# Performance work log

Measured on AMD Instinct MI355X. Metric: run time of the kernel, lower is better.

The kernel has to match this reference:

```python
import jax, jax.numpy as jnp
import numpy as np

N = 100000      # nodes
E = 1600000     # edges
IN = 64         # in_feats
H = 64          # h_feats
L = 4           # num_conv_layers
FC = 2          # num_fc_layers
G = 512         # num graphs in batch
EPS = 1e-5      # BatchNorm eps


def _bn(x, g, b):
    # training-mode BatchNorm1d: batch stats (biased variance), affine
    m = x.mean(axis=0)
    v = x.var(axis=0)
    return (x - m) * jax.lax.rsqrt(v + EPS) * g + b


def setup_inputs() -> dict:
    key = jax.random.key(0)
    ks = jax.random.split(key, 12)
    x = jax.random.normal(ks[0], (N, IN), jnp.float32)
    edge_index = jax.random.randint(ks[1], (2, E), 0, N)
    batch = jnp.sort(jax.random.randint(ks[2], (N,), 0, G))
    s_in = 1.0 / np.sqrt(IN)
    s_h = 1.0 / np.sqrt(H)
    return {
        "x": x,
        "edge_index": edge_index,
        "batch": batch,
        "bn_feat_g": jnp.ones((IN,), jnp.float32),
        "bn_feat_b": jnp.zeros((IN,), jnp.float32),
        "lin_feat_W": jax.random.normal(ks[3], (IN, H), jnp.float32) * s_in,
        "lin_feat_b": jnp.zeros((H,), jnp.float32),
        "bn_conv_g": jnp.ones((L, H), jnp.float32),
        "bn_conv_b": jnp.zeros((L, H), jnp.float32),
        "conv_W": jax.random.normal(ks[4], (L, H, H), jnp.float32) * s_h,
        "conv_b": jnp.zeros((L, H), jnp.float32),
        "bn_fc_g": jnp.ones((FC, H), jnp.float32),
        "bn_fc_b": jnp.zeros((FC, H), jnp.float32),
        "fc_W": jax.random.normal(ks[5], (FC, H, H), jnp.float32) * s_h,
        "fc_b": jnp.zeros((FC, H), jnp.float32),
        "bn_hid_g": jnp.ones((H,), jnp.float32),
        "bn_hid_b": jnp.zeros((H,), jnp.float32),
    }


def reference(x, edge_index, batch, bn_feat_g, bn_feat_b, lin_feat_W, lin_feat_b,
              bn_conv_g, bn_conv_b, conv_W, conv_b, bn_fc_g, bn_fc_b, fc_W, fc_b,
              bn_hid_g, bn_hid_b):
    # --- GCN symmetric normalization with self-loops (computed once) ---
    loop = jnp.arange(N)
    src = jnp.concatenate([edge_index[0], loop])   # source j
    dst = jnp.concatenate([edge_index[1], loop])   # target i
    deg = jax.ops.segment_sum(jnp.ones((E + N,), x.dtype), dst, num_segments=N)
    dinv = jnp.where(deg > 0, 1.0, 0.0) / jnp.sqrt(jnp.where(deg > 0, deg, 1.0))
    norm = dinv[src] * dinv[dst]                   # [E+N]

    # --- stem ---
    h = _bn(x, bn_feat_g, bn_feat_b)
    h = jax.nn.relu(h @ lin_feat_W + lin_feat_b)

    # --- stacked GCNConv + BN + ReLU + residual ---
    for i in range(L):
        h_ = _bn(h, bn_conv_g[i], bn_conv_b[i])
        m = h_ @ conv_W[i]                                    # [N,H]
        agg = jax.ops.segment_sum(norm[:, None] * m[src], dst, num_segments=N)
        h = h + jax.nn.relu(agg + conv_b[i])                  # residual=True

    # --- global add pool over graphs ---
    h = jax.ops.segment_sum(h, batch, num_segments=G)         # [G,H]

    # --- fc head ---
    for i in range(FC):
        h_ = _bn(h, bn_fc_g[i], bn_fc_b[i])
        h = jax.nn.relu(h_ @ fc_W[i] + fc_b[i])

    return _bn(h, bn_hid_g, bn_hid_b)
```

## Files before the change

### kernel.cpp

```cpp
#include <hip/hip_runtime.h>
#include <hip/hip_fp16.h>

#define NN 100000
#define EE 1600000
#define GG 512
#define NB ((NN + 255) / 256)

__global__ void deg_kernel(const int* __restrict__ ei, int* __restrict__ cnt, int E_) {
    int e = blockIdx.x * 256 + threadIdx.x;
    if (e < E_) atomicAdd(&cnt[ei[E_ + e]], 1);
}

__global__ void dinv_kernel(const int* __restrict__ cnt, float* __restrict__ dinv, int n) {
    int i = blockIdx.x * 256 + threadIdx.x;
    if (i < n) dinv[i] = rsqrtf((float)cnt[i] + 1.0f);
}

__global__ void blocksum(const int* __restrict__ cnt, int* __restrict__ bsum) {
    __shared__ int sh[256];
    int i = blockIdx.x * 256 + threadIdx.x;
    sh[threadIdx.x] = (i < NN) ? cnt[i] : 0;
    __syncthreads();
    for (int o = 128; o > 0; o >>= 1) {
        if (threadIdx.x < o) sh[threadIdx.x] += sh[threadIdx.x + o];
        __syncthreads();
    }
    if (threadIdx.x == 0) bsum[blockIdx.x] = sh[0];
}

__global__ void scan_bsum(int* __restrict__ bsum, int nb) {
    __shared__ int sh[512];
    int t = threadIdx.x;
    int v = (t < nb) ? bsum[t] : 0;
    int orig = v;
    sh[t] = v;
    __syncthreads();
    for (int o = 1; o < 512; o <<= 1) {
        int add = (t >= o) ? sh[t - o] : 0;
        __syncthreads();
        sh[t] += add;
        __syncthreads();
    }
    if (t < nb) bsum[t] = sh[t] - orig;
}

__global__ void scan_final(const int* __restrict__ cnt, const int* __restrict__ boff,
                           int* __restrict__ row_ptr, int* __restrict__ cursor) {
    __shared__ int sh[256];
    int i = blockIdx.x * 256 + threadIdx.x;
    int v = (i < NN) ? cnt[i] : 0;
    int orig = v;
    sh[threadIdx.x] = v;
    __syncthreads();
    for (int o = 1; o < 256; o <<= 1) {
        int add = (threadIdx.x >= o) ? sh[threadIdx.x - o] : 0;
        __syncthreads();
        sh[threadIdx.x] += add;
        __syncthreads();
    }
    if (i < NN) {
        int ex = boff[blockIdx.x] + sh[threadIdx.x] - orig;
        row_ptr[i] = ex;
        cursor[i] = ex;
    }
    if (i == 0) row_ptr[NN] = EE;
}

__global__ void fill_csr(const int* __restrict__ ei, const float* __restrict__ dinv,
                         int* __restrict__ cursor, int* __restrict__ csr_src,
                         float* __restrict__ csr_norm, int E_) {
    int e = blockIdx.x * 256 + threadIdx.x;
    if (e < E_) {
        int s = ei[e], d = ei[E_ + e];
        int pos = atomicAdd(&cursor[d], 1);
        csr_src[pos] = s;
        csr_norm[pos] = dinv[s] * dinv[d];
    }
}

__global__ void colstats(const float* __restrict__ A, int nrows, float* __restrict__ stats) {
    __shared__ float ssum[4][64];
    __shared__ float ssq[4][64];
    int tid = threadIdx.x;
    int col = tid & 63, rg = tid >> 6;
    float s = 0.f, q = 0.f;
    for (int r = blockIdx.x * 4 + rg; r < nrows; r += gridDim.x * 4) {
        float v = A[r * 64 + col];
        s += v;
        q = fmaf(v, v, q);
    }
    ssum[rg][col] = s; ssq[rg][col] = q;
    __syncthreads();
    if (tid < 64) {
        float ts = ssum[0][tid] + ssum[1][tid] + ssum[2][tid] + ssum[3][tid];
        float tq = ssq[0][tid] + ssq[1][tid] + ssq[2][tid] + ssq[3][tid];
        atomicAdd(&stats[tid], ts);
        atomicAdd(&stats[64 + tid], tq);
    }
}

__global__ void prep(const float* __restrict__ stats, float count,
                     const float* __restrict__ g, const float* __restrict__ b,
                     const float* __restrict__ W, const float* __restrict__ basebias,
                     float* __restrict__ Wp, float* __restrict__ bp) {
    int j = threadIdx.x;
    float acc = basebias ? basebias[j] : 0.f;
    for (int k = 0; k < 64; k++) {
        float mu  = stats[k] / count;
        float var = fmaxf(stats[64 + k] / count - mu * mu, 0.f);
        float rstd = rsqrtf(var + 1e-5f);
        float a = rstd * g[k];
        float w = W[k * 64 + j];
        Wp[k * 64 + j] = a * w;
        acc = fmaf(b[k] - mu * a, w, acc);
    }
    bp[j] = acc;
}

__global__ __launch_bounds__(256) void gemm64(const float* __restrict__ A,
                                              const float* __restrict__ Wp,
                                              const float* __restrict__ bp,
                                              float* __restrict__ C,
                                              __half* __restrict__ C16,
                                              int nrows, int dorelu,
                                              float* __restrict__ stats) {
    __shared__ float Ws[64 * 64];
    __shared__ float As[64 * 64];
    __shared__ float ssh[256];
    __shared__ float qsh[256];
    int tid = threadIdx.x;
    int row0 = blockIdx.x * 64;
    for (int i = tid; i < 4096; i += 256) {
        Ws[i] = Wp[i];
        int r = row0 + (i >> 6);
        As[i] = (r < nrows) ? A[row0 * 64 + i] : 0.f;
    }
    __syncthreads();
    int col = tid & 63;
    int rg = tid >> 6;
    float bcol = bp[col];
    float s = 0.f, q = 0.f;
    for (int rr = rg; rr < 64; rr += 4) {
        int r = row0 + rr;
        if (r >= nrows) break;
        float acc = bcol;
#pragma unroll
        for (int k = 0; k < 64; k++) acc = fmaf(As[rr * 64 + k], Ws[k * 64 + col], acc);
        float v = dorelu ? fmaxf(acc, 0.f) : acc;
        if (C)   C[r * 64 + col] = v;
        if (C16) C16[r * 64 + col] = __float2half(v);
        s += v;
        q = fmaf(v, v, q);
    }
    if (stats) {
        ssh[tid] = s; qsh[tid] = q;
        __syncthreads();
        if (tid < 64) {
            float ts = ssh[tid] + ssh[64 + tid] + ssh[128 + tid] + ssh[192 + tid];
            float tq = qsh[tid] + qsh[64 + tid] + qsh[128 + tid] + qsh[192 + tid];
            atomicAdd(&stats[tid], ts);
            atomicAdd(&stats[64 + tid], tq);
        }
    }
}

__device__ __forceinline__ void row4(const __half* __restrict__ base, int cl,
                                     float& x, float& y, float& z, float& w) {
    uint2 raw = ((const uint2*)base)[cl];
    __half2 h01 = *reinterpret_cast<const __half2*>(&raw.x);
    __half2 h23 = *reinterpret_cast<const __half2*>(&raw.y);
    float2 f01 = __half22float2(h01);
    float2 f23 = __half22float2(h23);
    x = f01.x; y = f01.y; z = f23.x; w = f23.y;
}

__global__ __launch_bounds__(256) void gather(const int* __restrict__ row_ptr,
                                              const int* __restrict__ csr_src,
                                              const float* __restrict__ csr_norm,
                                              const float* __restrict__ dinv,
                                              const __half* __restrict__ m,
                                              float* __restrict__ h,
                                              const float* __restrict__ cb,
                                              float* __restrict__ stats,
                                              float* __restrict__ pooled,
                                              const int* __restrict__ batch,
                                              int writeH) {
    int tid = threadIdx.x;
    int ng = tid >> 4;
    int cl = tid & 15;
    const float4* cb4 = (const float4*)cb;
    float4 cbv = cb4[cl];
    float sx = 0.f, sy = 0.f, sz = 0.f, sw = 0.f;
    float qx = 0.f, qy = 0.f, qz = 0.f, qw = 0.f;
    for (int i = blockIdx.x * 16 + ng; i < NN; i += gridDim.x * 16) {
        float di = dinv[i];
        float mx, my, mz, mw;
        row4(m + (size_t)i * 64, cl, mx, my, mz, mw);
        float d2 = di * di;
        float ax = d2 * mx, ay = d2 * my, az = d2 * mz, aw = d2 * mw;
        int e0 = row_ptr[i], e1 = row_ptr[i + 1];
        int e = e0;
        for (; e + 3 < e1; e += 4) {
            int s0 = csr_src[e + 0];
            int s1 = csr_src[e + 1];
            int s2 = csr_src[e + 2];
            int s3 = csr_src[e + 3];
            float w0 = csr_norm[e + 0];
            float w1 = csr_norm[e + 1];
            float w2 = csr_norm[e + 2];
            float w3 = csr_norm[e + 3];
            float x0, y0, z0, w0v, x1, y1, z1, w1v, x2, y2, z2, w2v, x3, y3, z3, w3v;
            row4(m + (size_t)s0 * 64, cl, x0, y0, z0, w0v);
            row4(m + (size_t)s1 * 64, cl, x1, y1, z1, w1v);
            row4(m + (size_t)s2 * 64, cl, x2, y2, z2, w2v);
            row4(m + (size_t)s3 * 64, cl, x3, y3, z3, w3v);
            ax = fmaf(w0, x0, ax); ay = fmaf(w0, y0, ay);
            az = fmaf(w0, z0, az); aw = fmaf(w0, w0v, aw);
            ax = fmaf(w1, x1, ax); ay = fmaf(w1, y1, ay);
            az = fmaf(w1, z1, az); aw = fmaf(w1, w1v, aw);
            ax = fmaf(w2, x2, ax); ay = fmaf(w2, y2, ay);
            az = fmaf(w2, z2, az); aw = fmaf(w2, w2v, aw);
            ax = fmaf(w3, x3, ax); ay = fmaf(w3, y3, ay);
            az = fmaf(w3, z3, az); aw = fmaf(w3, w3v, aw);
        }
        for (; e < e1; e++) {
            int s = csr_src[e];
            float w = csr_norm[e];
            float xs, ys, zs, wsv;
            row4(m + (size_t)s * 64, cl, xs, ys, zs, wsv);
            ax = fmaf(w, xs, ax);
            ay = fmaf(w, ys, ay);
            az = fmaf(w, zs, az);
            aw = fmaf(w, wsv, aw);
        }
        float4 hb = ((const float4*)(h + (size_t)i * 64))[cl];
        float nx = hb.x + fmaxf(ax + cbv.x, 0.f);
        float ny = hb.y + fmaxf(ay + cbv.y, 0.f);
        float nz = hb.z + fmaxf(az + cbv.z, 0.f);
        float nw = hb.w + fmaxf(aw + cbv.w, 0.f);
        if (writeH) {
            float4 o; o.x = nx; o.y = ny; o.z = nz; o.w = nw;
            ((float4*)(h + (size_t)i * 64))[cl] = o;
        }
        if (stats) {
            sx += nx; sy += ny; sz += nz; sw += nw;
            qx = fmaf(nx, nx, qx); qy = fmaf(ny, ny, qy);
            qz = fmaf(nz, nz, qz); qw = fmaf(nw, nw, qw);
        }
        if (pooled) {
            int g = batch[i];
            float* p = pooled + g * 64 + cl * 4;
            atomicAdd(p + 0, nx);
            atomicAdd(p + 1, ny);
            atomicAdd(p + 2, nz);
            atomicAdd(p + 3, nw);
        }
    }
    if (stats) {
        __shared__ float rs[256 * 4];
        __shared__ float rq[256 * 4];
        rs[tid * 4 + 0] = sx; rs[tid * 4 + 1] = sy; rs[tid * 4 + 2] = sz; rs[tid * 4 + 3] = sw;
        rq[tid * 4 + 0] = qx; rq[tid * 4 + 1] = qy; rq[tid * 4 + 2] = qz; rq[tid * 4 + 3] = qw;
        __syncthreads();
        if (tid < 64) {
            int cl2 = tid >> 2, k = tid & 3;
            float a = 0.f, b = 0.f;
            for (int g = 0; g < 16; g++) {
                a += rs[(g * 16 + cl2) * 4 + k];
                b += rq[(g * 16 + cl2) * 4 + k];
            }
            atomicAdd(&stats[tid], a);
            atomicAdd(&stats[64 + tid], b);
        }
    }
}

__global__ void bn_apply(const float* __restrict__ A, const float* __restrict__ stats, float count,
                         const float* __restrict__ g, const float* __restrict__ b,
                         float* __restrict__ out, int total) {
    int idx = blockIdx.x * 256 + threadIdx.x;
    if (idx < total) {
        int j = idx & 63;
        float mu  = stats[j] / count;
        float var = fmaxf(stats[64 + j] / count - mu * mu, 0.f);
        float rstd = rsqrtf(var + 1e-5f);
        out[idx] = (A[idx] - mu) * rstd * g[j] + b[j];
    }
}

extern "C" void kernel_launch(void* const* d_in, const int* in_sizes, int n_in,
                              void* d_out, int out_size, void* d_ws, size_t ws_size,
                              hipStream_t stream) {
    const float* x     = (const float*)d_in[0];
    const int*   ei    = (const int*)d_in[1];
    const int*   batch = (const int*)d_in[2];
    const float* bnfg  = (const float*)d_in[3];
    const float* bnfb  = (const float*)d_in[4];
    const float* linW  = (const float*)d_in[5];
    const float* linb  = (const float*)d_in[6];
    const float* bncg  = (const float*)d_in[7];
    const float* bncb  = (const float*)d_in[8];
    const float* convW = (const float*)d_in[9];
    const float* convb = (const float*)d_in[10];
    const float* bnfcg = (const float*)d_in[11];
    const float* bnfcb = (const float*)d_in[12];
    const float* fcW   = (const float*)d_in[13];
    const float* fcb   = (const float*)d_in[14];
    const float* bnhg  = (const float*)d_in[15];
    const float* bnhb  = (const float*)d_in[16];

    const int N64 = NN * 64;
    float* ws = (float*)d_ws;
    size_t o = 0;
    int*   cnt      = (int*)(ws + o);   o += 100352;
    float* dinv     = ws + o;           o += 100352;
    int*   row_ptr  = (int*)(ws + o);   o += 100352;
    int*   cursor   = (int*)(ws + o);   o += 100352;
    int*   bsum     = (int*)(ws + o);   o += 512;
    int*   csr_src  = (int*)(ws + o);   o += EE;
    float* csr_norm = ws + o;           o += EE;
    float* h        = ws + o;           o += N64;
    __half* m16     = (__half*)(ws + o); o += N64 / 2;
    float* statsA   = ws + o;           o += 128;
    float* statsB   = ws + o;           o += 128;
    float* Wp       = ws + o;           o += 4096;
    float* bp       = ws + o;           o += 64;
    float* pa       = ws + o;           o += GG * 64;
    float* pb       = ws + o;           o += GG * 64;

    hipMemsetAsync(cnt, 0, NN * sizeof(int), stream);
    deg_kernel<<<(EE + 255) / 256, 256, 0, stream>>>(ei, cnt, EE);
    dinv_kernel<<<NB, 256, 0, stream>>>(cnt, dinv, NN);
    blocksum<<<NB, 256, 0, stream>>>(cnt, bsum);
    scan_bsum<<<1, 512, 0, stream>>>(bsum, NB);
    scan_final<<<NB, 256, 0, stream>>>(cnt, bsum, row_ptr, cursor);
    fill_csr<<<(EE + 255) / 256, 256, 0, stream>>>(ei, dinv, cursor, csr_src, csr_norm, EE);

    hipMemsetAsync(statsA, 0, 512, stream);
    colstats<<<256, 256, 0, stream>>>(x, NN, statsA);
    prep<<<1, 64, 0, stream>>>(statsA, (float)NN, bnfg, bnfb, linW, linb, Wp, bp);
    hipMemsetAsync(statsB, 0, 512, stream);
    gemm64<<<(NN + 63) / 64, 256, 0, stream>>>(x, Wp, bp, h, nullptr, NN, 1, statsB);

    hipMemsetAsync(pa, 0, GG * 64 * sizeof(float), stream);
    float* cur = statsB; float* nxt = statsA;
    for (int l = 0; l < 4; l++) {
        prep<<<1, 64, 0, stream>>>(cur, (float)NN, bncg + 64 * l, bncb + 64 * l,
                                   convW + 4096 * l, nullptr, Wp, bp);
        gemm64<<<(NN + 63) / 64, 256, 0, stream>>>(h, Wp, bp, nullptr, m16, NN, 0, nullptr);
        if (l < 3) {
            hipMemsetAsync(nxt, 0, 512, stream);
            gather<<<2048, 256, 0, stream>>>(row_ptr, csr_src, csr_norm, dinv, m16, h,
                                             convb + 64 * l, nxt, nullptr, batch, 1);
        } else {
            gather<<<2048, 256, 0, stream>>>(row_ptr, csr_src, csr_norm, dinv, m16, h,
                                             convb + 64 * l, nullptr, pa, batch, 0);
        }
        float* t = cur; cur = nxt; nxt = t;
    }

    float* pin = pa; float* pout = pb;
    for (int i = 0; i < 2; i++) {
        hipMemsetAsync(statsA, 0, 512, stream);
        colstats<<<8, 256, 0, stream>>>(pin, GG, statsA);
        prep<<<1, 64, 0, stream>>>(statsA, (float)GG, bnfcg + 64 * i, bnfcb + 64 * i,
                                   fcW + 4096 * i, fcb + 64 * i, Wp, bp);
        gemm64<<<(GG + 63) / 64, 256, 0, stream>>>(pin, Wp, bp, pout, nullptr, GG, 1, nullptr);
        float* t = pin; pin = pout; pout = t;
    }

    hipMemsetAsync(statsA, 0, 512, stream);
    colstats<<<8, 256, 0, stream>>>(pin, GG, statsA);
    bn_apply<<<(GG * 64 + 255) / 256, 256, 0, stream>>>(pin, statsA, (float)GG, bnhg, bnhb,
                                                        (float*)d_out, GG * 64);
}
```

Baseline: 1.147 ms.

## Fuse BN prep into GEMM, store hidden state in fp16, drop csr_norm

Folds the BatchNorm-into-weights prep step into the GEMM kernel, so every block recomputes the scale and shift and the bias fold, and seven tiny single-block launches go away. The residual hidden state h is kept in fp16 instead of fp32, which halves its read/write traffic in the gather and GEMM kernels. The per-edge csr_norm array is dropped and recomputed in the gather as dinv[i]*dinv[src], trading a streamed array for an extra random gather. The cost is lower precision in the residual accumulation, more redundant work in each GEMM block, and extra random dinv reads.

```diff
diff --git a/kernel.cpp b/kernel.cpp
--- a/kernel.cpp
+++ b/kernel.cpp
@@ -66,15 +66,13 @@
     if (i == 0) row_ptr[NN] = EE;
 }
 
-__global__ void fill_csr(const int* __restrict__ ei, const float* __restrict__ dinv,
-                         int* __restrict__ cursor, int* __restrict__ csr_src,
-                         float* __restrict__ csr_norm, int E_) {
+__global__ void fill_csr(const int* __restrict__ ei, int* __restrict__ cursor,
+                         int* __restrict__ csr_src, int E_) {
     int e = blockIdx.x * 256 + threadIdx.x;
     if (e < E_) {
         int s = ei[e], d = ei[E_ + e];
         int pos = atomicAdd(&cursor[d], 1);
         csr_src[pos] = s;
-        csr_norm[pos] = dinv[s] * dinv[d];
     }
 }
 
@@ -99,46 +97,67 @@
     }
 }
 
-__global__ void prep(const float* __restrict__ stats, float count,
-                     const float* __restrict__ g, const float* __restrict__ b,
-                     const float* __restrict__ W, const float* __restrict__ basebias,
-                     float* __restrict__ Wp, float* __restrict__ bp) {
-    int j = threadIdx.x;
-    float acc = basebias ? basebias[j] : 0.f;
-    for (int k = 0; k < 64; k++) {
-        float mu  = stats[k] / count;
-        float var = fmaxf(stats[64 + k] / count - mu * mu, 0.f);
-        float rstd = rsqrtf(var + 1e-5f);
-        float a = rstd * g[k];
-        float w = W[k * 64 + j];
-        Wp[k * 64 + j] = a * w;
-        acc = fmaf(b[k] - mu * a, w, acc);
-    }
-    bp[j] = acc;
-}
-
-__global__ __launch_bounds__(256) void gemm64(const float* __restrict__ A,
-                                              const float* __restrict__ Wp,
-                                              const float* __restrict__ bp,
-                                              float* __restrict__ C,
-                                              __half* __restrict__ C16,
-                                              int nrows, int dorelu,
-                                              float* __restrict__ stats) {
+__global__ __launch_bounds__(256) void gemm64f(const float* __restrict__ A32,
+                                               const __half* __restrict__ A16,
+                                               const float* __restrict__ W,
+                                               const float* __restrict__ g,
+                                               const float* __restrict__ b,
+                                               const float* __restrict__ basebias,
+                                               const float* __restrict__ statsIn, float count,
+                                               float* __restrict__ C32,
+                                               __half* __restrict__ C16,
+                                               int nrows, int dorelu,
+                                               float* __restrict__ statsOut) {
     __shared__ float Ws[64 * 64];
     __shared__ float As[64 * 64];
+    __shared__ float afold[64];
+    __shared__ float cfold[64];
     __shared__ float ssh[256];
     __shared__ float qsh[256];
     int tid = threadIdx.x;
+    if (tid < 64) {
+        float mu  = statsIn[tid] / count;
+        float var = fmaxf(statsIn[64 + tid] / count - mu * mu, 0.f);
+        float rstd = rsqrtf(var + 1e-5f);
+        float a = rstd * g[tid];
+        afold[tid] = a;
+        cfold[tid] = b[tid] - mu * a;
+    }
+    __syncthreads();
     int row0 = blockIdx.x * 64;
-    for (int i = tid; i < 4096; i += 256) {
-        Ws[i] = Wp[i];
-        int r = row0 + (i >> 6);
-        As[i] = (r < nrows) ? A[row0 * 64 + i] : 0.f;
+    if (A32) {
+        for (int i = tid; i < 4096; i += 256) {
+            Ws[i] = afold[i >> 6] * W[i];
+            int r = row0 + (i >> 6);
+            As[i] = (r < nrows) ? A32[row0 * 64 + i] : 0.f;
+        }
+    } else {
+        for (int i = tid; i < 4096; i += 256) Ws[i] = afold[i >> 6] * W[i];
+        const uint4* Av = (const uint4*)(A16 + (size_t)row0 * 64);
+#pragma unroll
+        for (int p = 0; p < 2; p++) {
+            int idx = tid + 256 * p;
+            int r = row0 + (idx >> 3);
+            if (r < nrows) {
+                uint4 raw = Av[idx];
+                const __half2* hp = (const __half2*)&raw;
+#pragma unroll
+                for (int t = 0; t < 4; t++) {
+                    float2 v = __half22float2(hp[t]);
+                    As[idx * 8 + 2 * t]     = v.x;
+                    As[idx * 8 + 2 * t + 1] = v.y;
+                }
+            } else {
+#pragma unroll
+                for (int t = 0; t < 8; t++) As[idx * 8 + t] = 0.f;
+            }
+        }
     }
     __syncthreads();
     int col = tid & 63;
     int rg = tid >> 6;
-    float bcol = bp[col];
+    float bcol = basebias ? basebias[col] : 0.f;
+    for (int k = 0; k < 64; k++) bcol = fmaf(cfold[k], W[k * 64 + col], bcol);
     float s = 0.f, q = 0.f;
     for (int rr = rg; rr < 64; rr += 4) {
         int r = row0 + rr;
@@ -147,19 +166,19 @@
 #pragma unroll
         for (int k = 0; k < 64; k++) acc = fmaf(As[rr * 64 + k], Ws[k * 64 + col], acc);
         float v = dorelu ? fmaxf(acc, 0.f) : acc;
-        if (C)   C[r * 64 + col] = v;
+        if (C32) C32[r * 64 + col] = v;
         if (C16) C16[r * 64 + col] = __float2half(v);
         s += v;
         q = fmaf(v, v, q);
     }
-    if (stats) {
+    if (statsOut) {
         ssh[tid] = s; qsh[tid] = q;
         __syncthreads();
         if (tid < 64) {
             float ts = ssh[tid] + ssh[64 + tid] + ssh[128 + tid] + ssh[192 + tid];
             float tq = qsh[tid] + qsh[64 + tid] + qsh[128 + tid] + qsh[192 + tid];
-            atomicAdd(&stats[tid], ts);
-            atomicAdd(&stats[64 + tid], tq);
+            atomicAdd(&statsOut[tid], ts);
+            atomicAdd(&statsOut[64 + tid], tq);
         }
     }
 }
@@ -173,13 +192,21 @@
     float2 f23 = __half22float2(h23);
     x = f01.x; y = f01.y; z = f23.x; w = f23.y;
 }
+__device__ __forceinline__ void h4store(__half* __restrict__ base, int cl,
+                                        float x, float y, float z, float w) {
+    __half2 a = __float22half2_rn(make_float2(x, y));
+    __half2 b = __float22half2_rn(make_float2(z, w));
+    uint2 raw;
+    raw.x = *reinterpret_cast<unsigned*>(&a);
+    raw.y = *reinterpret_cast<unsigned*>(&b);
+    ((uint2*)base)[cl] = raw;
+}
 
 __global__ __launch_bounds__(256) void gather(const int* __restrict__ row_ptr,
                                               const int* __restrict__ csr_src,
-                                              const float* __restrict__ csr_norm,
                                               const float* __restrict__ dinv,
                                               const __half* __restrict__ m,
-                                              float* __restrict__ h,
+                                              __half* __restrict__ h,
                                               const float* __restrict__ cb,
                                               float* __restrict__ stats,
                                               float* __restrict__ pooled,
@@ -205,10 +232,10 @@
             int s1 = csr_src[e + 1];
             int s2 = csr_src[e + 2];
             int s3 = csr_src[e + 3];
-            float w0 = csr_norm[e + 0];
-            float w1 = csr_norm[e + 1];
-            float w2 = csr_norm[e + 2];
-            float w3 = csr_norm[e + 3];
+            float w0 = di * dinv[s0];
+            float w1 = di * dinv[s1];
+            float w2 = di * dinv[s2];
+            float w3 = di * dinv[s3];
             float x0, y0, z0, w0v, x1, y1, z1, w1v, x2, y2, z2, w2v, x3, y3, z3, w3v;
             row4(m + (size_t)s0 * 64, cl, x0, y0, z0, w0v);
             row4(m + (size_t)s1 * 64, cl, x1, y1, z1, w1v);
@@ -225,7 +252,7 @@
         }
         for (; e < e1; e++) {
             int s = csr_src[e];
-            float w = csr_norm[e];
+            float w = di * dinv[s];
             float xs, ys, zs, wsv;
             row4(m + (size_t)s * 64, cl, xs, ys, zs, wsv);
             ax = fmaf(w, xs, ax);
@@ -233,14 +260,14 @@
             az = fmaf(w, zs, az);
             aw = fmaf(w, wsv, aw);
         }
-        float4 hb = ((const float4*)(h + (size_t)i * 64))[cl];
-        float nx = hb.x + fmaxf(ax + cbv.x, 0.f);
-        float ny = hb.y + fmaxf(ay + cbv.y, 0.f);
-        float nz = hb.z + fmaxf(az + cbv.z, 0.f);
-        float nw = hb.w + fmaxf(aw + cbv.w, 0.f);
+        float hx, hy, hz, hw;
+        row4(h + (size_t)i * 64, cl, hx, hy, hz, hw);
+        float nx = hx + fmaxf(ax + cbv.x, 0.f);
+        float ny = hy + fmaxf(ay + cbv.y, 0.f);
+        float nz = hz + fmaxf(az + cbv.z, 0.f);
+        float nw = hw + fmaxf(aw + cbv.w, 0.f);
         if (writeH) {
-            float4 o; o.x = nx; o.y = ny; o.z = nz; o.w = nw;
-            ((float4*)(h + (size_t)i * 64))[cl] = o;
+            h4store(h + (size_t)i * 64, cl, nx, ny, nz, nw);
         }
         if (stats) {
             sx += nx; sy += ny; sz += nz; sw += nw;
@@ -318,13 +345,10 @@
     int*   cursor   = (int*)(ws + o);   o += 100352;
     int*   bsum     = (int*)(ws + o);   o += 512;
     int*   csr_src  = (int*)(ws + o);   o += EE;
-    float* csr_norm = ws + o;           o += EE;
-    float* h        = ws + o;           o += N64;
+    __half* h16     = (__half*)(ws + o); o += N64 / 2;
     __half* m16     = (__half*)(ws + o); o += N64 / 2;
     float* statsA   = ws + o;           o += 128;
     float* statsB   = ws + o;           o += 128;
-    float* Wp       = ws + o;           o += 4096;
-    float* bp       = ws + o;           o += 64;
     float* pa       = ws + o;           o += GG * 64;
     float* pb       = ws + o;           o += GG * 64;
 
@@ -334,26 +358,26 @@
     blocksum<<<NB, 256, 0, stream>>>(cnt, bsum);
     scan_bsum<<<1, 512, 0, stream>>>(bsum, NB);
     scan_final<<<NB, 256, 0, stream>>>(cnt, bsum, row_ptr, cursor);
-    fill_csr<<<(EE + 255) / 256, 256, 0, stream>>>(ei, dinv, cursor, csr_src, csr_norm, EE);
+    fill_csr<<<(EE + 255) / 256, 256, 0, stream>>>(ei, cursor, csr_src, EE);
 
     hipMemsetAsync(statsA, 0, 512, stream);
     colstats<<<256, 256, 0, stream>>>(x, NN, statsA);
-    prep<<<1, 64, 0, stream>>>(statsA, (float)NN, bnfg, bnfb, linW, linb, Wp, bp);
     hipMemsetAsync(statsB, 0, 512, stream);
-    gemm64<<<(NN + 63) / 64, 256, 0, stream>>>(x, Wp, bp, h, nullptr, NN, 1, statsB);
+    gemm64f<<<(NN + 63) / 64, 256, 0, stream>>>(x, nullptr, linW, bnfg, bnfb, linb,
+                                                statsA, (float)NN, nullptr, h16, NN, 1, statsB);
 
     hipMemsetAsync(pa, 0, GG * 64 * sizeof(float), stream);
     float* cur = statsB; float* nxt = statsA;
     for (int l = 0; l < 4; l++) {
-        prep<<<1, 64, 0, stream>>>(cur, (float)NN, bncg + 64 * l, bncb + 64 * l,
-                                   convW + 4096 * l, nullptr, Wp, bp);
-        gemm64<<<(NN + 63) / 64, 256, 0, stream>>>(h, Wp, bp, nullptr, m16, NN, 0, nullptr);
+        gemm64f<<<(NN + 63) / 64, 256, 0, stream>>>(nullptr, h16, convW + 4096 * l,
+                                                    bncg + 64 * l, bncb + 64 * l, nullptr,
+                                                    cur, (float)NN, nullptr, m16, NN, 0, nullptr);
         if (l < 3) {
             hipMemsetAsync(nxt, 0, 512, stream);
-            gather<<<2048, 256, 0, stream>>>(row_ptr, csr_src, csr_norm, dinv, m16, h,
+            gather<<<2048, 256, 0, stream>>>(row_ptr, csr_src, dinv, m16, h16,
                                              convb + 64 * l, nxt, nullptr, batch, 1);
         } else {
-            gather<<<2048, 256, 0, stream>>>(row_ptr, csr_src, csr_norm, dinv, m16, h,
+            gather<<<2048, 256, 0, stream>>>(row_ptr, csr_src, dinv, m16, h16,
                                              convb + 64 * l, nullptr, pa, batch, 0);
         }
         float* t = cur; cur = nxt; nxt = t;
@@ -363,9 +387,9 @@
     for (int i = 0; i < 2; i++) {
         hipMemsetAsync(statsA, 0, 512, stream);
         colstats<<<8, 256, 0, stream>>>(pin, GG, statsA);
-        prep<<<1, 64, 0, stream>>>(statsA, (float)GG, bnfcg + 64 * i, bnfcb + 64 * i,
-                                   fcW + 4096 * i, fcb + 64 * i, Wp, bp);
-        gemm64<<<(GG + 63) / 64, 256, 0, stream>>>(pin, Wp, bp, pout, nullptr, GG, 1, nullptr);
+        gemm64f<<<(GG + 63) / 64, 256, 0, stream>>>(pin, nullptr, fcW + 4096 * i,
+                                                    bnfcg + 64 * i, bnfcb + 64 * i, fcb + 64 * i,
+                                                    statsA, (float)GG, pout, nullptr, GG, 1, nullptr);
         float* t = pin; pin = pout; pout = t;
     }
 
```

Result: faster. 1.084 ms (-5.5%).
